# Kernel tuning notes

Hardware: AMD Instinct MI355X
Metric: run time of the kernel (lower is better)

## Reference

```python
import jax, jax.numpy as jnp
import numpy as np

B, S, D = 4, 2048, 768
H, R = 12, 8
Dh = D // H


def setup_inputs() -> dict:
    key = jax.random.key(0)
    ks = jax.random.split(key, 12)
    s_in = 1.0 / np.sqrt(D)
    s_r = 1.0 / np.sqrt(R)
    return {
        "x": jax.random.normal(ks[0], (B, S, D), jnp.float32),
        "Wq0": jax.random.normal(ks[1], (D, D), jnp.float32) * s_in,
        "Aq": jax.random.normal(ks[2], (D, R), jnp.float32) * s_in,
        "Bq": jax.random.normal(ks[3], (R, D), jnp.float32) * s_r,
        "Wk0": jax.random.normal(ks[4], (D, D), jnp.float32) * s_in,
        "Ak": jax.random.normal(ks[5], (D, R), jnp.float32) * s_in,
        "Bk": jax.random.normal(ks[6], (R, D), jnp.float32) * s_r,
        "Wv0": jax.random.normal(ks[7], (D, D), jnp.float32) * s_in,
        "Av": jax.random.normal(ks[8], (D, R), jnp.float32) * s_in,
        "Bv": jax.random.normal(ks[9], (R, D), jnp.float32) * s_r,
        "Wo": jax.random.normal(ks[10], (D, D), jnp.float32) * s_in,
        "bo": jnp.zeros((D,), jnp.float32),
    }


def _lora(x, W0, A, Bm):
    # x @ W0 + (x @ A) @ B  -- low-rank adapter on frozen W0
    return x @ W0 + (x @ A) @ Bm


def _split_heads(t):
    # [B,S,D] -> [B,H,S,Dh]
    return t.reshape(B, S, H, Dh).transpose(0, 2, 1, 3)


def reference(x, Wq0, Aq, Bq, Wk0, Ak, Bk, Wv0, Av, Bv, Wo, bo):
    q = _split_heads(_lora(x, Wq0, Aq, Bq))
    k = _split_heads(_lora(x, Wk0, Ak, Bk))
    v = _split_heads(_lora(x, Wv0, Av, Bv))
    scale = 1.0 / jnp.sqrt(jnp.asarray(Dh, x.dtype))
    scores = jnp.einsum("bhqd,bhkd->bhqk", q, k) * scale  # [B,H,S,S]
    weights = jax.nn.softmax(scores, axis=-1)
    attn = jnp.einsum("bhqk,bhkd->bhqd", weights, v)
    concat = attn.transpose(0, 2, 1, 3).reshape(B, S, D)
    return concat @ Wo + bo
```

## Files before the change

### kernel.cpp

```cpp
#include <hip/hip_runtime.h>
#include <hip/hip_bf16.h>


typedef unsigned short ushort_t;
typedef __bf16 bf16x8 __attribute__((ext_vector_type(8)));
typedef float f32x4 __attribute__((ext_vector_type(4)));
typedef unsigned short ushort8 __attribute__((ext_vector_type(8)));
typedef unsigned short ushort4_t __attribute__((ext_vector_type(4)));
typedef __attribute__((address_space(1))) unsigned int gu32;
typedef __attribute__((address_space(3))) unsigned int lu32;

__device__ __forceinline__ unsigned short f2bf(float f) {
  unsigned int u = __builtin_bit_cast(unsigned int, f);
  u += 0x7fffu + ((u >> 16) & 1u);
  return (unsigned short)(u >> 16);
}

__device__ __forceinline__ void gld_lds16(const void* g, void* s) {
  __builtin_amdgcn_global_load_lds((gu32*)(unsigned long long)g,
                                   (lu32*)(unsigned int)(unsigned long long)s,
                                   16, 0, 0);
}

__device__ __forceinline__ f32x4 mfma16(bf16x8 a, bf16x8 b, f32x4 c) {
  return __builtin_amdgcn_mfma_f32_16x16x32_bf16(a, b, c, 0, 0, 0);
}

__global__ __launch_bounds__(256) void prep_weights(
    const float* __restrict__ Wq0, const float* __restrict__ Aq, const float* __restrict__ Bq,
    const float* __restrict__ Wk0, const float* __restrict__ Ak, const float* __restrict__ Bk,
    const float* __restrict__ Wv0, const float* __restrict__ Av, const float* __restrict__ Bv,
    const float* __restrict__ Wo,
    ushort_t* __restrict__ WeffT, ushort_t* __restrict__ WoT)
{
  __shared__ float tile[32][33];
  __shared__ float tA[32][8];
  __shared__ float tB[8][32];
  const int mat = blockIdx.y;
  const int kt = blockIdx.x / 24, nt = blockIdx.x % 24;
  const int k0 = kt * 32, n0 = nt * 32;
  const float* W0 = (mat == 0) ? Wq0 : (mat == 1) ? Wk0 : (mat == 2) ? Wv0 : Wo;
  const float* Am = (mat == 0) ? Aq : (mat == 1) ? Ak : (mat == 2) ? Av : nullptr;
  const float* Bm = (mat == 0) ? Bq : (mat == 1) ? Bk : (mat == 2) ? Bv : nullptr;
  const int tid = threadIdx.x;
#pragma unroll
  for (int i = 0; i < 4; i++) {
    int rr = i * 8 + (tid >> 5), c = tid & 31;
    tile[rr][c] = W0[(k0 + rr) * 768 + n0 + c];
  }
  if (Am) {
    tA[tid >> 3][tid & 7] = Am[(k0 + (tid >> 3)) * 8 + (tid & 7)];
    tB[tid >> 5][tid & 31] = Bm[(tid >> 5) * 768 + n0 + (tid & 31)];
  }
  __syncthreads();
#pragma unroll
  for (int i = 0; i < 4; i++) {
    int kk = tid & 31;
    int nn = i * 8 + (tid >> 5);
    float val = tile[kk][nn];
    if (Am) {
#pragma unroll
      for (int rr = 0; rr < 8; rr++) val += tA[kk][rr] * tB[rr][nn];
    }
    int n = n0 + nn, kg = k0 + kk;
    if (mat < 3) WeffT[((long)mat * 768 + n) * 768 + kg] = f2bf(val);
    else         WoT[(long)n * 768 + kg] = f2bf(val);
  }
}

__global__ __launch_bounds__(256) void cast_x(const float* __restrict__ x,
                                              ushort_t* __restrict__ xb)
{
  long i = (long)blockIdx.x * 256 + threadIdx.x;
  const float4* xp = (const float4*)x;
  float4 a = xp[i * 2], c = xp[i * 2 + 1];
  ushort8 rv;
  rv[0] = f2bf(a.x); rv[1] = f2bf(a.y); rv[2] = f2bf(a.z); rv[3] = f2bf(a.w);
  rv[4] = f2bf(c.x); rv[5] = f2bf(c.y); rv[6] = f2bf(c.z); rv[7] = f2bf(c.w);
  *(ushort8*)&xb[i * 8] = rv;
}

template <int MODE>
__global__ __launch_bounds__(256) void gemm_bt(
    const ushort_t* __restrict__ A, const ushort_t* __restrict__ Bt,
    ushort_t* __restrict__ q, ushort_t* __restrict__ kbuf, ushort_t* __restrict__ vt,
    float* __restrict__ out, const float* __restrict__ bo)
{
  constexpr int K = 768;
  __shared__ ushort_t As[128 * 64];
  __shared__ ushort_t Bs[128 * 64];
  const int tid = threadIdx.x;
  const int l = tid & 63, w = tid >> 6;
  const int wm = w >> 1, wn = w & 1;
  const int lr = l & 15, lg = l >> 4;
  const long rowBase = (long)blockIdx.x * 128;
  const long colBase = (long)blockIdx.y * 128;
  f32x4 acc[4][4] = {};

  for (int k0 = 0; k0 < K; k0 += 64) {
    __syncthreads();
#pragma unroll
    for (int i = 0; i < 4; i++) {
      int ci = i * 256 + tid;
      gld_lds16(A + (rowBase + (ci >> 3)) * K + k0 + (ci & 7) * 8, &As[ci * 8]);
    }
#pragma unroll
    for (int i = 0; i < 4; i++) {
      int ci = i * 256 + tid;
      gld_lds16(Bt + (colBase + (ci >> 3)) * K + k0 + (ci & 7) * 8, &Bs[ci * 8]);
    }
    asm volatile("s_waitcnt vmcnt(0)" ::: "memory");
    __syncthreads();
#pragma unroll
    for (int ks = 0; ks < 2; ks++) {
      bf16x8 af[4], bf[4];
#pragma unroll
      for (int m = 0; m < 4; m++)
        af[m] = *(const bf16x8*)&As[(wm * 64 + m * 16 + lr) * 64 + ks * 32 + lg * 8];
#pragma unroll
      for (int n = 0; n < 4; n++)
        bf[n] = *(const bf16x8*)&Bs[(wn * 64 + n * 16 + lr) * 64 + ks * 32 + lg * 8];
#pragma unroll
      for (int m = 0; m < 4; m++)
#pragma unroll
        for (int n = 0; n < 4; n++)
          acc[m][n] = mfma16(af[m], bf[n], acc[m][n]);
    }
  }

  if (MODE == 0) {
    const int mat = (int)(colBase / 768);
    if (mat == 2) {
      const long cb = colBase - 1536;
#pragma unroll
      for (int m = 0; m < 4; m++) {
        long srow = rowBase + wm * 64 + m * 16 + lg * 4;
        long b = srow >> 11, s = srow & 2047;
#pragma unroll
        for (int n = 0; n < 4; n++) {
          long col = cb + wn * 64 + n * 16 + lr;
          ushort4_t pk;
#pragma unroll
          for (int r = 0; r < 4; r++) pk[r] = f2bf(acc[m][n][r]);
          *(ushort4_t*)&vt[(b * 768 + col) * 2048 + s] = pk;
        }
      }
    } else {
      ushort_t* dst = (mat == 0) ? q : kbuf;
      const float scl = (mat == 0) ? 0.125f * 1.4426950408889634f : 1.0f;
      const long cb = colBase - (long)mat * 768;
#pragma unroll
      for (int m = 0; m < 4; m++)
#pragma unroll
        for (int n = 0; n < 4; n++) {
          long col = cb + wn * 64 + n * 16 + lr;
#pragma unroll
          for (int r = 0; r < 4; r++) {
            long row = rowBase + wm * 64 + m * 16 + lg * 4 + r;
            dst[row * 768 + col] = f2bf(acc[m][n][r] * scl);
          }
        }
    }
  } else {
#pragma unroll
    for (int m = 0; m < 4; m++)
#pragma unroll
      for (int n = 0; n < 4; n++) {
        long col = colBase + wn * 64 + n * 16 + lr;
        float bv = bo[col];
#pragma unroll
        for (int r = 0; r < 4; r++) {
          long row = rowBase + wm * 64 + m * 16 + lg * 4 + r;
          out[row * 768 + col] = acc[m][n][r] + bv;
        }
      }
  }
}

__global__ __launch_bounds__(256) void attn_fwd(
    const ushort_t* __restrict__ Q, const ushort_t* __restrict__ Kg,
    const ushort_t* __restrict__ VtG, ushort_t* __restrict__ O)
{
  constexpr int D = 768, S = 2048;
  __shared__ ushort_t Ks[2][64 * 64];
  __shared__ ushort_t Vs[2][64 * 64];
  __shared__ ushort_t Ps[4][32 * 64];
  const int tid = threadIdx.x;
  const int l = tid & 63, w = tid >> 6;
  const int lr = l & 15, lg = l >> 4;
  const int i = blockIdx.x;
  const int xcd = i & 7, j = i >> 3;
  const int bh = xcd * 6 + (j >> 4);
  const int q0 = (j & 15) * 128;
  const int b = bh / 12, h = bh % 12;
  const ushort_t* Qb = Q + (long)b * S * D + h * 64;
  const ushort_t* Kb = Kg + (long)b * S * D + h * 64;
  const ushort_t* Vb = VtG + ((long)b * 768 + h * 64) * S;

  bf16x8 qf[2][2];
#pragma unroll
  for (int m = 0; m < 2; m++)
#pragma unroll
    for (int ks = 0; ks < 2; ks++)
      qf[m][ks] = *(const bf16x8*)&Qb[(long)(q0 + w * 32 + m * 16 + lr) * D + ks * 32 + lg * 8];

  bf16x8 ones;
#pragma unroll
  for (int e = 0; e < 8; e++) ones[e] = (__bf16)1.0f;

  f32x4 o[2][4], o1[2];
#pragma unroll
  for (int m = 0; m < 2; m++) {
    o1[m] = (f32x4){0.f, 0.f, 0.f, 0.f};
#pragma unroll
    for (int n = 0; n < 4; n++) o[m][n] = (f32x4){0.f, 0.f, 0.f, 0.f};
  }

  const int swz = lr & 7;

  auto STAGE = [&](int t, int bi) {
    const int kbase = t * 64;
#pragma unroll
    for (int it = 0; it < 2; it++) {
      int ci = it * 256 + tid;
      int r = ci >> 3, bp = ci & 7;
      gld_lds16(Kb + (long)(kbase + r) * D + ((bp ^ (r & 7)) * 8), &Ks[bi][ci * 8]);
    }
#pragma unroll
    for (int it = 0; it < 2; it++) {
      int ci = it * 256 + tid;
      int d = ci >> 3, bp = ci & 7;
      gld_lds16(Vb + (long)d * S + kbase + ((bp ^ (d & 7)) * 8), &Vs[bi][ci * 8]);
    }
  };

  STAGE(0, 0);

  for (int kt = 0; kt < 32; kt++) {
    const int cur = kt & 1;
    STAGE((kt + 1) & 31, cur ^ 1);
    asm volatile("s_waitcnt vmcnt(4)" ::: "memory");
    __builtin_amdgcn_s_barrier();

    const ushort_t* ksb = &Ks[cur][0];
    const ushort_t* vsb = &Vs[cur][0];

    f32x4 s[2][4];
#pragma unroll
    for (int m = 0; m < 2; m++)
#pragma unroll
      for (int n = 0; n < 4; n++) s[m][n] = (f32x4){0.f, 0.f, 0.f, 0.f};
    __builtin_amdgcn_s_setprio(1);
#pragma unroll
    for (int ks = 0; ks < 2; ks++) {
#pragma unroll
      for (int n = 0; n < 4; n++) {
        int key = n * 16 + lr;
        bf16x8 kf = *(const bf16x8*)&ksb[key * 64 + (((ks * 4 + lg) ^ swz) * 8)];
#pragma unroll
        for (int m = 0; m < 2; m++)
          s[m][n] = mfma16(qf[m][ks], kf, s[m][n]);
      }
    }
    __builtin_amdgcn_s_setprio(0);

#pragma unroll
    for (int m = 0; m < 2; m++)
#pragma unroll
      for (int n = 0; n < 4; n++)
#pragma unroll
        for (int r = 0; r < 4; r++) {
          float p = __builtin_amdgcn_exp2f(s[m][n][r]);
          int ro = m * 16 + lg * 4 + r;
          int ch = (n * 2 + (lr >> 3)) ^ ((ro >> 1) & 7);
          Ps[w][ro * 64 + ch * 8 + (lr & 7)] = f2bf(p);
        }

#pragma unroll
    for (int ks = 0; ks < 2; ks++) {
      bf16x8 pf[2], vf[4];
#pragma unroll
      for (int m = 0; m < 2; m++)
        pf[m] = *(const bf16x8*)&Ps[w][(m * 16 + lr) * 64 + (((ks * 4 + lg) ^ ((lr >> 1) & 7)) * 8)];
#pragma unroll
      for (int n = 0; n < 4; n++) {
        int d = n * 16 + lr;
        vf[n] = *(const bf16x8*)&vsb[d * 64 + (((ks * 4 + lg) ^ swz) * 8)];
      }
      __builtin_amdgcn_s_setprio(1);
#pragma unroll
      for (int m = 0; m < 2; m++) {
        o1[m] = mfma16(pf[m], ones, o1[m]);
#pragma unroll
        for (int n = 0; n < 4; n++)
          o[m][n] = mfma16(pf[m], vf[n], o[m][n]);
      }
      __builtin_amdgcn_s_setprio(0);
    }

    asm volatile("" ::: "memory");
    __builtin_amdgcn_s_barrier();
  }

#pragma unroll
  for (int m = 0; m < 2; m++) {
    float inv[4];
#pragma unroll
    for (int r = 0; r < 4; r++) inv[r] = 1.0f / o1[m][r];
#pragma unroll
    for (int n = 0; n < 4; n++)
#pragma unroll
      for (int r = 0; r < 4; r++) {
        float val = o[m][n][r] * inv[r];
        O[((long)b * S + q0 + w * 32 + m * 16 + lg * 4 + r) * D + h * 64 + n * 16 + lr] = f2bf(val);
      }
  }
}

extern "C" void kernel_launch(void* const* d_in, const int* in_sizes, int n_in,
                              void* d_out, int out_size, void* d_ws, size_t ws_size,
                              hipStream_t stream)
{
  const float* x   = (const float*)d_in[0];
  const float* Wq0 = (const float*)d_in[1];
  const float* Aq  = (const float*)d_in[2];
  const float* Bq  = (const float*)d_in[3];
  const float* Wk0 = (const float*)d_in[4];
  const float* Ak  = (const float*)d_in[5];
  const float* Bk  = (const float*)d_in[6];
  const float* Wv0 = (const float*)d_in[7];
  const float* Av  = (const float*)d_in[8];
  const float* Bv  = (const float*)d_in[9];
  const float* Wo  = (const float*)d_in[10];
  const float* bo  = (const float*)d_in[11];
  float* out = (float*)d_out;

  char* ws = (char*)d_ws;
  const long SZ = 8192L * 768 * 2;
  ushort_t* xb    = (ushort_t*)(ws);
  ushort_t* Qb    = (ushort_t*)(ws + SZ);
  ushort_t* Kb    = (ushort_t*)(ws + 2 * SZ);
  ushort_t* Vt    = (ushort_t*)(ws + 3 * SZ);
  ushort_t* At    = (ushort_t*)(ws + 4 * SZ);
  ushort_t* WeffT = (ushort_t*)(ws + 5 * SZ);
  ushort_t* WoT   = (ushort_t*)(ws + 5 * SZ + 2304L * 768 * 2);

  hipLaunchKernelGGL(prep_weights, dim3(576, 4), dim3(256), 0, stream,
                     Wq0, Aq, Bq, Wk0, Ak, Bk, Wv0, Av, Bv, Wo, WeffT, WoT);
  hipLaunchKernelGGL(cast_x, dim3(3072), dim3(256), 0, stream, x, xb);
  hipLaunchKernelGGL((gemm_bt<0>), dim3(64, 18), dim3(256), 0, stream,
                     xb, WeffT, Qb, Kb, Vt, (float*)nullptr, (const float*)nullptr);
  hipLaunchKernelGGL(attn_fwd, dim3(768), dim3(256), 0, stream, Qb, Kb, Vt, At);
  hipLaunchKernelGGL((gemm_bt<1>), dim3(64, 6), dim3(256), 0, stream,
                     At, WoT, (ushort_t*)nullptr, (ushort_t*)nullptr, (ushort_t*)nullptr,
                     out, bo);
}
```

Baseline: 180.1 us.

## Switch attention to 32x32 MFMA and keep P in registers via transposed scores

```diff
diff --git a/kernel.cpp b/kernel.cpp
--- a/kernel.cpp
+++ b/kernel.cpp
@@ -5,8 +5,10 @@
 typedef unsigned short ushort_t;
 typedef __bf16 bf16x8 __attribute__((ext_vector_type(8)));
 typedef float f32x4 __attribute__((ext_vector_type(4)));
+typedef float f32x16 __attribute__((ext_vector_type(16)));
 typedef unsigned short ushort8 __attribute__((ext_vector_type(8)));
 typedef unsigned short ushort4_t __attribute__((ext_vector_type(4)));
+typedef unsigned int uint4v __attribute__((ext_vector_type(4)));
 typedef __attribute__((address_space(1))) unsigned int gu32;
 typedef __attribute__((address_space(3))) unsigned int lu32;
 
@@ -22,8 +24,24 @@
                                    16, 0, 0);
 }
 
+__device__ __forceinline__ void gld_lds4(const void* g, void* s) {
+  __builtin_amdgcn_global_load_lds((gu32*)(unsigned long long)g,
+                                   (lu32*)(unsigned int)(unsigned long long)s,
+                                   4, 0, 0);
+}
+
 __device__ __forceinline__ f32x4 mfma16(bf16x8 a, bf16x8 b, f32x4 c) {
   return __builtin_amdgcn_mfma_f32_16x16x32_bf16(a, b, c, 0, 0, 0);
+}
+
+__device__ __forceinline__ f32x16 mfma32(bf16x8 a, bf16x8 b, f32x16 c) {
+  return __builtin_amdgcn_mfma_f32_32x32x16_bf16(a, b, c, 0, 0, 0);
+}
+
+__device__ __forceinline__ unsigned int cvtpk(float a, float b) {
+  unsigned int r;
+  asm("v_cvt_pk_bf16_f32 %0, %1, %2" : "=v"(r) : "v"(a), "v"(b));
+  return r;
 }
 
 __global__ __launch_bounds__(256) void prep_weights(
@@ -184,10 +202,9 @@
   constexpr int D = 768, S = 2048;
   __shared__ ushort_t Ks[2][64 * 64];
   __shared__ ushort_t Vs[2][64 * 64];
-  __shared__ ushort_t Ps[4][32 * 64];
   const int tid = threadIdx.x;
   const int l = tid & 63, w = tid >> 6;
-  const int lr = l & 15, lg = l >> 4;
+  const int q32 = l & 31, hi = l >> 5;
   const int i = blockIdx.x;
   const int xcd = i & 7, j = i >> 3;
   const int bh = xcd * 6 + (j >> 4);
@@ -197,41 +214,47 @@
   const ushort_t* Kb = Kg + (long)b * S * D + h * 64;
   const ushort_t* Vb = VtG + ((long)b * 768 + h * 64) * S;
 
-  bf16x8 qf[2][2];
-#pragma unroll
-  for (int m = 0; m < 2; m++)
-#pragma unroll
-    for (int ks = 0; ks < 2; ks++)
-      qf[m][ks] = *(const bf16x8*)&Qb[(long)(q0 + w * 32 + m * 16 + lr) * D + ks * 32 + lg * 8];
+  bf16x8 qf[4];
+  {
+    const ushort_t* qrow = Qb + (long)(q0 + w * 32 + q32) * D + hi * 8;
+#pragma unroll
+    for (int ks = 0; ks < 4; ks++) qf[ks] = *(const bf16x8*)&qrow[ks * 16];
+  }
+
+  int koff[2];
+#pragma unroll
+  for (int it = 0; it < 2; it++) {
+    int ci = it * 256 + tid, r = ci >> 3, bp = ci & 7;
+    koff[it] = r * D + ((bp ^ (r & 7)) * 8);
+  }
+  int voff[8];
+#pragma unroll
+  for (int it = 0; it < 8; it++) {
+    int vi = it * 256 + tid;
+    int d = vi >> 5, c_l = (vi >> 2) & 7, slot = vi & 3;
+    int c = c_l ^ (d & 7);
+    int p = c * 8 + slot * 2;
+    int a = p >> 4, hp = (p >> 3) & 1, jj = p & 7;
+    int key = 32 * (a >> 1) + 16 * (a & 1) + 8 * (jj >> 2) + (jj & 3) + 4 * hp;
+    voff[it] = d * S + key;
+  }
 
   bf16x8 ones;
 #pragma unroll
   for (int e = 0; e < 8; e++) ones[e] = (__bf16)1.0f;
 
-  f32x4 o[2][4], o1[2];
-#pragma unroll
-  for (int m = 0; m < 2; m++) {
-    o1[m] = (f32x4){0.f, 0.f, 0.f, 0.f};
-#pragma unroll
-    for (int n = 0; n < 4; n++) o[m][n] = (f32x4){0.f, 0.f, 0.f, 0.f};
-  }
-
-  const int swz = lr & 7;
-
-  auto STAGE = [&](int t, int bi) {
-    const int kbase = t * 64;
-#pragma unroll
-    for (int it = 0; it < 2; it++) {
-      int ci = it * 256 + tid;
-      int r = ci >> 3, bp = ci & 7;
-      gld_lds16(Kb + (long)(kbase + r) * D + ((bp ^ (r & 7)) * 8), &Ks[bi][ci * 8]);
-    }
-#pragma unroll
-    for (int it = 0; it < 2; it++) {
-      int ci = it * 256 + tid;
-      int d = ci >> 3, bp = ci & 7;
-      gld_lds16(Vb + (long)d * S + kbase + ((bp ^ (d & 7)) * 8), &Vs[bi][ci * 8]);
-    }
+  f32x16 oA = {}, oB = {}, osum = {};
+  const int swz = q32 & 7;
+
+  auto STAGE = [&](int kt, int bi) {
+    const ushort_t* kp = Kb + (long)kt * 64 * D;
+#pragma unroll
+    for (int it = 0; it < 2; it++)
+      gld_lds16(kp + koff[it], &Ks[bi][(it * 256 + tid) * 8]);
+    const ushort_t* vp = Vb + kt * 64;
+#pragma unroll
+    for (int it = 0; it < 8; it++)
+      gld_lds4(vp + voff[it], &Vs[bi][(it * 256 + tid) * 2]);
   };
 
   STAGE(0, 0);
@@ -239,81 +262,63 @@
   for (int kt = 0; kt < 32; kt++) {
     const int cur = kt & 1;
     STAGE((kt + 1) & 31, cur ^ 1);
-    asm volatile("s_waitcnt vmcnt(4)" ::: "memory");
+    asm volatile("s_waitcnt vmcnt(10)" ::: "memory");
     __builtin_amdgcn_s_barrier();
 
     const ushort_t* ksb = &Ks[cur][0];
     const ushort_t* vsb = &Vs[cur][0];
 
-    f32x4 s[2][4];
-#pragma unroll
-    for (int m = 0; m < 2; m++)
-#pragma unroll
-      for (int n = 0; n < 4; n++) s[m][n] = (f32x4){0.f, 0.f, 0.f, 0.f};
+    f32x16 s0 = {}, s1 = {};
     __builtin_amdgcn_s_setprio(1);
 #pragma unroll
-    for (int ks = 0; ks < 2; ks++) {
-#pragma unroll
-      for (int n = 0; n < 4; n++) {
-        int key = n * 16 + lr;
-        bf16x8 kf = *(const bf16x8*)&ksb[key * 64 + (((ks * 4 + lg) ^ swz) * 8)];
-#pragma unroll
-        for (int m = 0; m < 2; m++)
-          s[m][n] = mfma16(qf[m][ks], kf, s[m][n]);
-      }
+    for (int ks = 0; ks < 4; ks++) {
+      int ch = ((ks * 2 + hi) ^ swz) * 8;
+      bf16x8 kf0 = *(const bf16x8*)&ksb[q32 * 64 + ch];
+      bf16x8 kf1 = *(const bf16x8*)&ksb[(32 + q32) * 64 + ch];
+      s0 = mfma32(kf0, qf[ks], s0);
+      s1 = mfma32(kf1, qf[ks], s1);
     }
     __builtin_amdgcn_s_setprio(0);
 
-#pragma unroll
-    for (int m = 0; m < 2; m++)
-#pragma unroll
-      for (int n = 0; n < 4; n++)
-#pragma unroll
-        for (int r = 0; r < 4; r++) {
-          float p = __builtin_amdgcn_exp2f(s[m][n][r]);
-          int ro = m * 16 + lg * 4 + r;
-          int ch = (n * 2 + (lr >> 3)) ^ ((ro >> 1) & 7);
-          Ps[w][ro * 64 + ch * 8 + (lr & 7)] = f2bf(p);
-        }
-
-#pragma unroll
-    for (int ks = 0; ks < 2; ks++) {
-      bf16x8 pf[2], vf[4];
-#pragma unroll
-      for (int m = 0; m < 2; m++)
-        pf[m] = *(const bf16x8*)&Ps[w][(m * 16 + lr) * 64 + (((ks * 4 + lg) ^ ((lr >> 1) & 7)) * 8)];
-#pragma unroll
-      for (int n = 0; n < 4; n++) {
-        int d = n * 16 + lr;
-        vf[n] = *(const bf16x8*)&vsb[d * 64 + (((ks * 4 + lg) ^ swz) * 8)];
-      }
-      __builtin_amdgcn_s_setprio(1);
-#pragma unroll
-      for (int m = 0; m < 2; m++) {
-        o1[m] = mfma16(pf[m], ones, o1[m]);
-#pragma unroll
-        for (int n = 0; n < 4; n++)
-          o[m][n] = mfma16(pf[m], vf[n], o[m][n]);
-      }
-      __builtin_amdgcn_s_setprio(0);
-    }
+    unsigned int pw[16];
+#pragma unroll
+    for (int u = 0; u < 8; u++) {
+      float a0 = __builtin_amdgcn_exp2f(s0[2 * u]);
+      float a1 = __builtin_amdgcn_exp2f(s0[2 * u + 1]);
+      pw[u] = cvtpk(a0, a1);
+    }
+#pragma unroll
+    for (int u = 0; u < 8; u++) {
+      float a0 = __builtin_amdgcn_exp2f(s1[2 * u]);
+      float a1 = __builtin_amdgcn_exp2f(s1[2 * u + 1]);
+      pw[8 + u] = cvtpk(a0, a1);
+    }
+
+    __builtin_amdgcn_s_setprio(1);
+#pragma unroll
+    for (int ks = 0; ks < 4; ks++) {
+      uint4v w4 = {pw[4 * ks], pw[4 * ks + 1], pw[4 * ks + 2], pw[4 * ks + 3]};
+      bf16x8 pa = __builtin_bit_cast(bf16x8, w4);
+      int ch = ((ks * 2 + hi) ^ swz) * 8;
+      bf16x8 vf0 = *(const bf16x8*)&vsb[q32 * 64 + ch];
+      bf16x8 vf1 = *(const bf16x8*)&vsb[(32 + q32) * 64 + ch];
+      oA = mfma32(pa, vf0, oA);
+      oB = mfma32(pa, vf1, oB);
+      osum = mfma32(pa, ones, osum);
+    }
+    __builtin_amdgcn_s_setprio(0);
 
     asm volatile("" ::: "memory");
     __builtin_amdgcn_s_barrier();
   }
 
 #pragma unroll
-  for (int m = 0; m < 2; m++) {
-    float inv[4];
-#pragma unroll
-    for (int r = 0; r < 4; r++) inv[r] = 1.0f / o1[m][r];
-#pragma unroll
-    for (int n = 0; n < 4; n++)
-#pragma unroll
-      for (int r = 0; r < 4; r++) {
-        float val = o[m][n][r] * inv[r];
-        O[((long)b * S + q0 + w * 32 + m * 16 + lg * 4 + r) * D + h * 64 + n * 16 + lr] = f2bf(val);
-      }
+  for (int reg = 0; reg < 16; reg++) {
+    int row = (reg & 3) + 8 * (reg >> 2) + 4 * hi;
+    float inv = 1.0f / osum[reg];
+    long base = ((long)b * S + q0 + w * 32 + row) * D + h * 64 + q32;
+    O[base] = f2bf(oA[reg] * inv);
+    O[base + 32] = f2bf(oB[reg] * inv);
   }
 }
 
```

Result: faster. 174.9 us (-2.9%).
